# Kernel optimization log

Measured on AMD Instinct MI355X. Metric: run time of the kernel, lower is better.

## Reference

```python
import jax, jax.numpy as jnp
import numpy as np

DIM = 512
N = 131072


def _linear_params(key, dim):
    # torch nn.Linear default init: U(-1/sqrt(in), 1/sqrt(in)) for W and b
    kw, kb = jax.random.split(key)
    bound = 1.0 / np.sqrt(dim)
    W = jax.random.uniform(kw, (dim, dim), jnp.float32, -bound, bound)
    b = jax.random.uniform(kb, (dim,), jnp.float32, -bound, bound)
    return W, b


def setup_inputs() -> dict:
    key = jax.random.key(0)
    ks = jax.random.split(key, 8)
    x = jax.random.normal(ks[0], (N, DIM), jnp.float32)
    h = jax.random.normal(ks[1], (N, DIM), jnp.float32)
    W_rx, b_rx = _linear_params(ks[2], DIM)
    W_rh, b_rh = _linear_params(ks[3], DIM)
    W_zx, b_zx = _linear_params(ks[4], DIM)
    W_zh, b_zh = _linear_params(ks[5], DIM)
    W_nx, b_nx = _linear_params(ks[6], DIM)
    W_nh, b_nh = _linear_params(ks[7], DIM)
    return {
        "x": x, "h": h,
        "W_rx": W_rx, "b_rx": b_rx, "W_rh": W_rh, "b_rh": b_rh,
        "W_zx": W_zx, "b_zx": b_zx, "W_zh": W_zh, "b_zh": b_zh,
        "W_nx": W_nx, "b_nx": b_nx, "W_nh": W_nh, "b_nh": b_nh,
    }


def reference(x, h, W_rx, b_rx, W_rh, b_rh, W_zx, b_zx, W_zh, b_zh,
              W_nx, b_nx, W_nh, b_nh):
    # torch Linear: y = x @ W.T + b  (W stored [out, in])
    r = jax.nn.sigmoid(x @ W_rx.T + b_rx + h @ W_rh.T + b_rh)
    z = jax.nn.sigmoid(x @ W_zx.T + b_zx + h @ W_zh.T + b_zh)
    n = jnp.tanh(x @ W_nx.T + b_nx + (r * h) @ W_nh.T + b_nh)
    return (1.0 - z) * n + z * h
```

## Files before the change

### kernel.cpp

```cpp
#include <hip/hip_runtime.h>

#define DIM 512
#define NROWS 131072

typedef __attribute__((ext_vector_type(8))) __bf16 bf16x8;
typedef __attribute__((ext_vector_type(4))) float f32x4;

__device__ __forceinline__ unsigned short f2bf(float f) {
  unsigned u = __builtin_bit_cast(unsigned, f);
  return (unsigned short)((u + 0x7FFFu + ((u >> 16) & 1u)) >> 16);
}
__device__ __forceinline__ float bf2f(unsigned short u) {
  return __builtin_bit_cast(float, (unsigned)u << 16);
}

__device__ __forceinline__ f32x4 mfma16(bf16x8 a, bf16x8 b, f32x4 c) {
  return __builtin_amdgcn_mfma_f32_16x16x32_bf16(a, b, c, 0, 0, 0);
}

__device__ __forceinline__ float sigmoid_fast(float v) {
  return 1.0f / (1.0f + __expf(-v));
}
__device__ __forceinline__ float tanh_fast(float v) {
  float e = __expf(2.0f * v);
  return 1.0f - 2.0f / (e + 1.0f);
}

__device__ __forceinline__ void gl2lds(const unsigned char* g, unsigned char* l) {
  __builtin_amdgcn_global_load_lds(
      (const __attribute__((address_space(1))) unsigned int*)g,
      (__attribute__((address_space(3))) unsigned int*)l, 16, 0, 0);
}

__global__ void prepack_weights(const float* __restrict__ W0, const float* __restrict__ W1,
                                const float* __restrict__ W2, const float* __restrict__ W3,
                                const float* __restrict__ W4, const float* __restrict__ W5,
                                unsigned short* __restrict__ out) {
  int idx = blockIdx.x * 256 + threadIdx.x;
  int e = idx & 7;
  int l = (idx >> 3) & 63;
  int c = (idx >> 9) & 31;
  int f = (idx >> 14) & 15;
  int g = idx >> 18;
  const float* W = (g == 0) ? W0 : (g == 1) ? W1 : (g == 2) ? W2
                 : (g == 3) ? W3 : (g == 4) ? W4 : W5;
  int row = c * 16 + (l & 15);
  int kk  = f * 32 + ((l >> 4) << 3) + e;
  out[idx] = f2bf(W[row * DIM + kk]);
}

#define RH_OFF 65536
#define X_OFF  131072
#define LDS_BYTES 139264

__global__ __launch_bounds__(512, 1)
void gru_fused(const float* __restrict__ x, const float* __restrict__ h,
               const unsigned char* __restrict__ WB,
               const float* __restrict__ b_rx, const float* __restrict__ b_rh,
               const float* __restrict__ b_zx, const float* __restrict__ b_zh,
               const float* __restrict__ b_nx, const float* __restrict__ b_nh,
               float* __restrict__ out) {
  __shared__ __align__(1024) unsigned char lds[LDS_BYTES];

  const int tid  = threadIdx.x;
  const int lane = tid & 63;
  const int w    = tid >> 6;
  const int cfg0 = w * 4;
  const int row0 = blockIdx.x * 64;
  const int lr   = lane & 15;
  const int lk   = lane >> 4;

  auto stageChunk = [&](int g, int f, int dstOff) {
    const unsigned char* src = WB + (size_t)(g * 16 + f) * 32768;
#pragma unroll
    for (int it = 0; it < 4; ++it) {
      int o = (it * 512 + tid) * 16;
      gl2lds(src + o, &lds[dstOff + o]);
    }
  };

  float4 xreg;
  auto loadX = [&](int f) {
    int row = tid >> 3, kq = tid & 7;
    xreg = *(const float4*)(x + (size_t)(row0 + row) * DIM + f * 32 + kq * 4);
  };
  auto writeX = [&](int f) {
    int row = tid >> 3, kq = tid & 7;
    union { unsigned short us[4]; uint2 v; } p;
    p.us[0] = f2bf(xreg.x); p.us[1] = f2bf(xreg.y);
    p.us[2] = f2bf(xreg.z); p.us[3] = f2bf(xreg.w);
    *(uint2*)&lds[X_OFF + (f & 1) * 4096 + (row >> 4) * 1024
                  + ((kq >> 1) * 16 + (row & 15)) * 16 + (kq & 1) * 8] = p.v;
  };

  auto gateStage = [&](int abase, int bbase, f32x4 (&A)[4][4]) {
    bf16x8 af[4], bfr[4];
#pragma unroll
    for (int rf = 0; rf < 4; ++rf)
      af[rf] = *(const bf16x8*)&lds[abase + rf * 1024 + lane * 16];
#pragma unroll
    for (int cf = 0; cf < 4; ++cf)
      bfr[cf] = *(const bf16x8*)&lds[bbase + (cfg0 + cf) * 1024 + lane * 16];
#pragma unroll
    for (int rf = 0; rf < 4; ++rf)
#pragma unroll
      for (int cf = 0; cf < 4; ++cf)
        A[rf][cf] = mfma16(af[rf], bfr[cf], A[rf][cf]);
  };

  f32x4 accR[4][4] = {}, accZ[4][4] = {};

#pragma unroll
  for (int it = 0; it < 16; ++it) {
    int i = tid + it * 512;
    int row = i >> 7, kf4 = i & 127;
    int k = kf4 * 4;
    float4 hv4 = *(const float4*)(h + (size_t)(row0 + row) * DIM + k);
    union { unsigned short us[4]; uint2 v; } p;
    p.us[0] = f2bf(hv4.x); p.us[1] = f2bf(hv4.y);
    p.us[2] = f2bf(hv4.z); p.us[3] = f2bf(hv4.w);
    *(uint2*)&lds[(k >> 5) * 4096 + (row >> 4) * 1024
                  + (((k >> 3) & 3) * 16 + (row & 15)) * 16 + (k & 4) * 2] = p.v;
  }
  loadX(0); writeX(0);
  stageChunk(0, 0, RH_OFF);
  __syncthreads();

#pragma unroll 1
  for (int f = 0; f < 16; ++f) {
    const int xoff = X_OFF + (f & 1) * 4096;
    const int hoff = f * 4096;
    stageChunk(1, f, RH_OFF + 32768);
    if (f < 15) loadX(f + 1);
    gateStage(xoff, RH_OFF, accR);
    __syncthreads();
    stageChunk(2, f, RH_OFF);
    gateStage(xoff, RH_OFF + 32768, accZ);
    __syncthreads();
    stageChunk(3, f, RH_OFF + 32768);
    if (f < 15) writeX(f + 1);
    gateStage(hoff, RH_OFF, accR);
    __syncthreads();
    if (f < 15) stageChunk(0, f + 1, RH_OFF);
    gateStage(hoff, RH_OFF + 32768, accZ);
    __syncthreads();
  }

#pragma unroll
  for (int cf = 0; cf < 4; ++cf) {
    const int col  = (cfg0 + cf) * 16 + lr;
    const float bs = b_rx[col] + b_rh[col];
    const int fcol  = col >> 5;
    const int l2b   = ((col >> 3) & 3) * 16;
    const int ebyte = (col & 7) * 2;
#pragma unroll
    for (int rf = 0; rf < 4; ++rf) {
#pragma unroll
      for (int j = 0; j < 4; ++j) {
        const int rsub = lk * 4 + j;
        unsigned short hu = *(const unsigned short*)
            &lds[fcol * 4096 + rf * 1024 + (l2b + rsub) * 16 + ebyte];
        float rv = sigmoid_fast(accR[rf][cf][j] + bs);
        *(unsigned short*)
            &lds[RH_OFF + fcol * 4096 + rf * 1024 + (l2b + rsub) * 16 + ebyte]
            = f2bf(rv * bf2f(hu));
      }
    }
  }
  __syncthreads();

  f32x4 accN[4][4] = {};
  loadX(0); writeX(0);
  stageChunk(4, 0, 0);
  __syncthreads();
#pragma unroll 1
  for (int f = 0; f < 16; ++f) {
    const int xoff = X_OFF + (f & 1) * 4096;
    stageChunk(5, f, 32768);
    if (f < 15) loadX(f + 1);
    gateStage(xoff, 0, accN);
    __syncthreads();
    if (f < 15) { stageChunk(4, f + 1, 0); writeX(f + 1); }
    gateStage(RH_OFF + f * 4096, 32768, accN);
    __syncthreads();
  }

#pragma unroll
  for (int cf = 0; cf < 4; ++cf) {
    const int col  = (cfg0 + cf) * 16 + lr;
    const float bn = b_nx[col] + b_nh[col];
    const float bz = b_zx[col] + b_zh[col];
#pragma unroll
    for (int rf = 0; rf < 4; ++rf) {
#pragma unroll
      for (int j = 0; j < 4; ++j) {
        const int row = rf * 16 + lk * 4 + j;
        const size_t off = (size_t)(row0 + row) * DIM + col;
        float hv = h[off];
        float nv = tanh_fast(accN[rf][cf][j] + bn);
        float zv = sigmoid_fast(accZ[rf][cf][j] + bz);
        out[off] = (1.0f - zv) * nv + zv * hv;
      }
    }
  }
}

extern "C" void kernel_launch(void* const* d_in, const int* in_sizes, int n_in,
                              void* d_out, int out_size, void* d_ws, size_t ws_size,
                              hipStream_t stream) {
  const float* x    = (const float*)d_in[0];
  const float* h    = (const float*)d_in[1];
  const float* W_rx = (const float*)d_in[2];
  const float* b_rx = (const float*)d_in[3];
  const float* W_rh = (const float*)d_in[4];
  const float* b_rh = (const float*)d_in[5];
  const float* W_zx = (const float*)d_in[6];
  const float* b_zx = (const float*)d_in[7];
  const float* W_zh = (const float*)d_in[8];
  const float* b_zh = (const float*)d_in[9];
  const float* W_nx = (const float*)d_in[10];
  const float* b_nx = (const float*)d_in[11];
  const float* W_nh = (const float*)d_in[12];
  const float* b_nh = (const float*)d_in[13];

  unsigned short* wpack = (unsigned short*)d_ws;

  prepack_weights<<<6144, 256, 0, stream>>>(W_rx, W_zx, W_rh, W_zh, W_nx, W_nh, wpack);
  gru_fused<<<NROWS / 64, 512, 0, stream>>>(x, h, (const unsigned char*)wpack,
                                            b_rx, b_rh, b_zx, b_zh, b_nx, b_nh,
                                            (float*)d_out);
}
```

Before: 766.2 us.

## Split fused GRU into two tiled GEMM kernels with r*h workspace

Replaces the single fused kernel (64-row blocks, one block per CU, full weight restaging per block) with two conventional tiled GEMM kernels. The first computes the r and z gates over 128x128 output tiles with double-buffered LDS, XOR-swizzled fp32 A tiles and a grid swizzle. It writes r*h as bf16 to a workspace and z into the output buffer. The second computes n from x and the r*h workspace and combines it with z and h. This should raise occupancy and improve weight reuse, at the cost of extra global traffic for the r*h and z intermediates and fp32-to-bf16 conversion during LDS reads.

```diff
diff --git a/kernel.cpp b/kernel.cpp
--- a/kernel.cpp
+++ b/kernel.cpp
@@ -5,6 +5,8 @@
 
 typedef __attribute__((ext_vector_type(8))) __bf16 bf16x8;
 typedef __attribute__((ext_vector_type(4))) float f32x4;
+
+union BF8 { unsigned short us[8]; bf16x8 v; };
 
 __device__ __forceinline__ unsigned short f2bf(float f) {
   unsigned u = __builtin_bit_cast(unsigned, f);
@@ -47,6 +49,250 @@
   int row = c * 16 + (l & 15);
   int kk  = f * 32 + ((l >> 4) << 3) + e;
   out[idx] = f2bf(W[row * DIM + kk]);
+}
+
+
+__global__ __launch_bounds__(256, 3)
+void gemm_rz(const float* __restrict__ x, const float* __restrict__ h,
+             const unsigned char* __restrict__ WB,
+             const float* __restrict__ b_rx, const float* __restrict__ b_rh,
+             const float* __restrict__ b_zx, const float* __restrict__ b_zh,
+             unsigned short* __restrict__ rhws, float* __restrict__ zout) {
+  __shared__ __align__(1024) unsigned char ldsA[2][16384];
+  __shared__ __align__(1024) unsigned char ldsB[2][8192];
+
+  const int tid = threadIdx.x;
+  const int lane = tid & 63;
+  const int w = tid >> 6;
+  const int lr = lane & 15, lk = lane >> 4;
+  const int row0w = (w & 1) * 64;
+  const int cfw = (w >> 1) * 4;
+
+  const int bid = blockIdx.x;
+  const int swz = (bid & 7) * 1024 + (bid >> 3);
+  const int panel = swz >> 3;
+  const int n = swz & 7;
+  const int row0 = panel * 128;
+  const bool isR = (n < 4);
+  const int gx = isR ? 0 : 1, gh = isR ? 2 : 3;
+  const int c0 = (n & 3) * 8;
+
+  f32x4 acc[4][4] = {};
+
+  auto stageA = [&](int f, int buf) {
+    const float* src = (f < 16) ? x : h;
+    const int fk = f & 15;
+#pragma unroll
+    for (int it = 0; it < 4; ++it) {
+      int d = it * 4096 + tid * 16;
+      int row = d >> 7;
+      int u = (d >> 4) & 7;
+      const unsigned char* s =
+          (const unsigned char*)(src + (size_t)(row0 + row) * DIM + fk * 32)
+          + (((u ^ (row & 7)) & 7) << 4);
+      gl2lds(s, &ldsA[buf][d]);
+    }
+  };
+  auto stageB = [&](int g, int fk, int buf) {
+    const unsigned char* s = WB + ((size_t)((g * 16 + fk) * 32 + c0) << 10);
+#pragma unroll
+    for (int it = 0; it < 2; ++it) {
+      int d = it * 4096 + tid * 16;
+      gl2lds(s + d, &ldsB[buf][d]);
+    }
+  };
+  auto compute = [&](int buf) {
+    bf16x8 bfr[4], af[4];
+#pragma unroll
+    for (int cf = 0; cf < 4; ++cf)
+      bfr[cf] = *(const bf16x8*)&ldsB[buf][(cfw + cf) * 1024 + lane * 16];
+#pragma unroll
+    for (int rf = 0; rf < 4; ++rf) {
+      int rfr = row0w + rf * 16 + lr;
+      int u0 = lk * 2;
+      f32x4 a0 = *(const f32x4*)&ldsA[buf][rfr * 128 + (((u0) ^ (rfr & 7)) << 4)];
+      f32x4 a1 = *(const f32x4*)&ldsA[buf][rfr * 128 + (((u0 + 1) ^ (rfr & 7)) << 4)];
+      union { __bf16 e[8]; bf16x8 v; } cv;
+      cv.e[0] = (__bf16)a0[0]; cv.e[1] = (__bf16)a0[1];
+      cv.e[2] = (__bf16)a0[2]; cv.e[3] = (__bf16)a0[3];
+      cv.e[4] = (__bf16)a1[0]; cv.e[5] = (__bf16)a1[1];
+      cv.e[6] = (__bf16)a1[2]; cv.e[7] = (__bf16)a1[3];
+      af[rf] = cv.v;
+    }
+#pragma unroll
+    for (int rf = 0; rf < 4; ++rf)
+#pragma unroll
+      for (int cf = 0; cf < 4; ++cf)
+        acc[rf][cf] = mfma16(af[rf], bfr[cf], acc[rf][cf]);
+  };
+
+  stageA(0, 0); stageB(gx, 0, 0);
+  __syncthreads();
+#pragma unroll 1
+  for (int f = 0; f < 32; ++f) {
+    int buf = f & 1;
+    if (f < 31) {
+      int fn = f + 1;
+      stageA(fn, buf ^ 1);
+      stageB((fn < 16) ? gx : gh, fn & 15, buf ^ 1);
+    }
+    compute(buf);
+    __syncthreads();
+  }
+
+  const float* bx = isR ? b_rx : b_zx;
+  const float* bh = isR ? b_rh : b_zh;
+  const int coltile = (n & 3) * 128;
+#pragma unroll
+  for (int cf = 0; cf < 4; ++cf) {
+    int cg = coltile + (cfw + cf) * 16 + lr;
+    float bsum = bx[cg] + bh[cg];
+#pragma unroll
+    for (int rf = 0; rf < 4; ++rf) {
+#pragma unroll
+      for (int j = 0; j < 4; ++j) {
+        int row = row0 + row0w + rf * 16 + lk * 4 + j;
+        size_t off = (size_t)row * DIM + cg;
+        float v = acc[rf][cf][j] + bsum;
+        if (isR) {
+          float rv = sigmoid_fast(v);
+          rhws[off] = f2bf(rv * h[off]);
+        } else {
+          zout[off] = sigmoid_fast(v);
+        }
+      }
+    }
+  }
+}
+
+__global__ __launch_bounds__(256, 3)
+void gemm_n(const float* __restrict__ x, const float* __restrict__ h,
+            const unsigned char* __restrict__ WB,
+            const unsigned short* __restrict__ rhws,
+            const float* __restrict__ b_nx, const float* __restrict__ b_nh,
+            float* __restrict__ out) {
+  __shared__ __align__(1024) unsigned char ldsA[2][16384];
+  __shared__ __align__(1024) unsigned char ldsB[2][8192];
+
+  const int tid = threadIdx.x;
+  const int lane = tid & 63;
+  const int w = tid >> 6;
+  const int lr = lane & 15, lk = lane >> 4;
+  const int row0w = (w & 1) * 64;
+  const int cfw = (w >> 1) * 4;
+
+  const int bid = blockIdx.x;
+  const int swz = (bid & 7) * 512 + (bid >> 3);
+  const int panel = swz >> 2;
+  const int n = swz & 3;
+  const int row0 = panel * 128;
+  const int c0 = n * 8;
+
+  f32x4 acc[4][4] = {};
+
+  auto stageA = [&](int fk, int buf) {
+#pragma unroll
+    for (int it = 0; it < 4; ++it) {
+      int d = it * 4096 + tid * 16;
+      int row = d >> 7;
+      int u = (d >> 4) & 7;
+      const unsigned char* s =
+          (const unsigned char*)(x + (size_t)(row0 + row) * DIM + fk * 32)
+          + (((u ^ (row & 7)) & 7) << 4);
+      gl2lds(s, &ldsA[buf][d]);
+    }
+  };
+  auto stageRH = [&](int f2, int buf) {
+    const unsigned char* base = (const unsigned char*)rhws;
+#pragma unroll
+    for (int it = 0; it < 2; ++it) {
+      int d = it * 4096 + tid * 16;
+      int row = d >> 6;
+      int u = (d >> 4) & 3;
+      const unsigned char* s = base + (size_t)(row0 + row) * 1024 + f2 * 64
+                               + ((u ^ ((row >> 1) & 3)) << 4);
+      gl2lds(s, &ldsA[buf][d]);
+    }
+  };
+  auto stageB = [&](int g, int fk, int buf) {
+    const unsigned char* s = WB + ((size_t)((g * 16 + fk) * 32 + c0) << 10);
+#pragma unroll
+    for (int it = 0; it < 2; ++it) {
+      int d = it * 4096 + tid * 16;
+      gl2lds(s + d, &ldsB[buf][d]);
+    }
+  };
+  auto loadB = [&](int buf, bf16x8 (&bfr)[4]) {
+#pragma unroll
+    for (int cf = 0; cf < 4; ++cf)
+      bfr[cf] = *(const bf16x8*)&ldsB[buf][(cfw + cf) * 1024 + lane * 16];
+  };
+  auto domfma = [&](bf16x8 (&af)[4], bf16x8 (&bfr)[4]) {
+#pragma unroll
+    for (int rf = 0; rf < 4; ++rf)
+#pragma unroll
+      for (int cf = 0; cf < 4; ++cf)
+        acc[rf][cf] = mfma16(af[rf], bfr[cf], acc[rf][cf]);
+  };
+  auto computeX = [&](int buf) {
+    bf16x8 bfr[4], af[4];
+    loadB(buf, bfr);
+#pragma unroll
+    for (int rf = 0; rf < 4; ++rf) {
+      int rfr = row0w + rf * 16 + lr;
+      int u0 = lk * 2;
+      f32x4 a0 = *(const f32x4*)&ldsA[buf][rfr * 128 + (((u0) ^ (rfr & 7)) << 4)];
+      f32x4 a1 = *(const f32x4*)&ldsA[buf][rfr * 128 + (((u0 + 1) ^ (rfr & 7)) << 4)];
+      union { __bf16 e[8]; bf16x8 v; } cv;
+      cv.e[0] = (__bf16)a0[0]; cv.e[1] = (__bf16)a0[1];
+      cv.e[2] = (__bf16)a0[2]; cv.e[3] = (__bf16)a0[3];
+      cv.e[4] = (__bf16)a1[0]; cv.e[5] = (__bf16)a1[1];
+      cv.e[6] = (__bf16)a1[2]; cv.e[7] = (__bf16)a1[3];
+      af[rf] = cv.v;
+    }
+    domfma(af, bfr);
+  };
+  auto computeRH = [&](int buf) {
+    bf16x8 bfr[4], af[4];
+    loadB(buf, bfr);
+#pragma unroll
+    for (int rf = 0; rf < 4; ++rf) {
+      int rfr = row0w + rf * 16 + lr;
+      af[rf] = *(const bf16x8*)&ldsA[buf][rfr * 64 + ((lk ^ ((rfr >> 1) & 3)) << 4)];
+    }
+    domfma(af, bfr);
+  };
+
+  stageA(0, 0); stageB(4, 0, 0);
+  __syncthreads();
+#pragma unroll 1
+  for (int f = 0; f < 32; ++f) {
+    int buf = f & 1;
+    if (f < 31) {
+      int fn = f + 1;
+      if (fn < 16) { stageA(fn, buf ^ 1);      stageB(4, fn, buf ^ 1); }
+      else         { stageRH(fn - 16, buf ^ 1); stageB(5, fn - 16, buf ^ 1); }
+    }
+    if (f < 16) computeX(buf); else computeRH(buf);
+    __syncthreads();
+  }
+
+#pragma unroll
+  for (int cf = 0; cf < 4; ++cf) {
+    int cg = n * 128 + (cfw + cf) * 16 + lr;
+    float bsum = b_nx[cg] + b_nh[cg];
+#pragma unroll
+    for (int rf = 0; rf < 4; ++rf) {
+#pragma unroll
+      for (int j = 0; j < 4; ++j) {
+        int row = row0 + row0w + rf * 16 + lk * 4 + j;
+        size_t off = (size_t)row * DIM + cg;
+        float nv = tanh_fast(acc[rf][cf][j] + bsum);
+        float zv = out[off];
+        out[off] = (1.0f - zv) * nv + zv * h[off];
+      }
+    }
+  }
 }
 
 #define RH_OFF 65536
@@ -223,10 +469,22 @@
   const float* W_nh = (const float*)d_in[12];
   const float* b_nh = (const float*)d_in[13];
 
-  unsigned short* wpack = (unsigned short*)d_ws;
+  unsigned char* ws = (unsigned char*)d_ws;
+  unsigned short* wpack = (unsigned short*)ws;
 
   prepack_weights<<<6144, 256, 0, stream>>>(W_rx, W_zx, W_rh, W_zh, W_nx, W_nh, wpack);
-  gru_fused<<<NROWS / 64, 512, 0, stream>>>(x, h, (const unsigned char*)wpack,
-                                            b_rx, b_rh, b_zx, b_zh, b_nx, b_nh,
-                                            (float*)d_out);
-}
+
+  const size_t need = (4ull << 20) + (size_t)NROWS * DIM * 2;
+  if (ws_size >= need) {
+    unsigned short* rhws = (unsigned short*)(ws + (4ull << 20));
+    gemm_rz<<<8192, 256, 0, stream>>>(x, h, (const unsigned char*)wpack,
+                                      b_rx, b_rh, b_zx, b_zh,
+                                      rhws, (float*)d_out);
+    gemm_n<<<4096, 256, 0, stream>>>(x, h, (const unsigned char*)wpack,
+                                     rhws, b_nx, b_nh, (float*)d_out);
+  } else {
+    gru_fused<<<NROWS / 64, 512, 0, stream>>>(x, h, (const unsigned char*)wpack,
+                                              b_rx, b_rh, b_zx, b_zh, b_nx, b_nh,
+                                              (float*)d_out);
+  }
+}
```

New measurement: 1.178 ms. 1.54x slower.

## Pre-convert x to bf16 and stream it via async LDS loads with vmcnt waits

Applied to the files above, without the earlier changes.

A new pre-kernel converts x to bf16 in workspace, and the main kernel stages x tiles straight into LDS with global_load_lds in pairs of k-chunks, instead of a register load, convert and LDS write. The __syncthreads calls are replaced by explicit s_waitcnt vmcnt counts plus bare s_barrier, so weight and x loads can stay in flight across barriers. The aim is to take x conversion and register round-trips off the critical path and overlap loads with MFMA work. In exchange it adds an extra pass over x (read fp32, write bf16) and relies on fragile hand-counted vmcnt values.

```diff
diff --git a/kernel.cpp b/kernel.cpp
--- a/kernel.cpp
+++ b/kernel.cpp
@@ -26,7 +26,7 @@
   return 1.0f - 2.0f / (e + 1.0f);
 }
 
-__device__ __forceinline__ void gl2lds(const unsigned char* g, unsigned char* l) {
+__device__ __forceinline__ void gl2lds(const void* g, void* l) {
   __builtin_amdgcn_global_load_lds(
       (const __attribute__((address_space(1))) unsigned int*)g,
       (__attribute__((address_space(3))) unsigned int*)l, 16, 0, 0);
@@ -49,12 +49,23 @@
   out[idx] = f2bf(W[row * DIM + kk]);
 }
 
-#define RH_OFF 65536
-#define X_OFF  131072
-#define LDS_BYTES 139264
+__global__ void prep_x(const float* __restrict__ x, unsigned short* __restrict__ xb) {
+  size_t i = (size_t)(blockIdx.x * 256 + threadIdx.x) * 8;
+  float4 a0 = *(const float4*)(x + i);
+  float4 a1 = *(const float4*)(x + i + 4);
+  union { unsigned short us[8]; uint4 v; } p;
+  p.us[0] = f2bf(a0.x); p.us[1] = f2bf(a0.y); p.us[2] = f2bf(a0.z); p.us[3] = f2bf(a0.w);
+  p.us[4] = f2bf(a1.x); p.us[5] = f2bf(a1.y); p.us[6] = f2bf(a1.z); p.us[7] = f2bf(a1.w);
+  *(uint4*)(xb + i) = p.v;
+}
+
+#define BOFF 65536
+#define XOFF 131072
+#define LDS_BYTES 147456
 
 __global__ __launch_bounds__(512, 1)
 void gru_fused(const float* __restrict__ x, const float* __restrict__ h,
+               const unsigned short* __restrict__ xb,
                const unsigned char* __restrict__ WB,
                const float* __restrict__ b_rx, const float* __restrict__ b_rh,
                const float* __restrict__ b_zx, const float* __restrict__ b_zh,
@@ -70,29 +81,20 @@
   const int lr   = lane & 15;
   const int lk   = lane >> 4;
 
-  auto stageChunk = [&](int g, int f, int dstOff) {
+  auto stageB = [&](int g, int f, int dst) {
     const unsigned char* src = WB + (size_t)(g * 16 + f) * 32768;
 #pragma unroll
     for (int it = 0; it < 4; ++it) {
       int o = (it * 512 + tid) * 16;
-      gl2lds(src + o, &lds[dstOff + o]);
+      gl2lds(src + o, &lds[dst + o]);
     }
   };
-
-  float4 xreg;
-  auto loadX = [&](int f) {
-    int row = tid >> 3, kq = tid & 7;
-    xreg = *(const float4*)(x + (size_t)(row0 + row) * DIM + f * 32 + kq * 4);
+  auto stageXpair = [&](int p) {
+    int fh = tid >> 8, rf = (tid >> 6) & 3, l = tid & 63;
+    const unsigned short* src = xb + (size_t)(row0 + rf * 16 + (l & 15)) * DIM
+                                + p * 64 + fh * 32 + (l >> 4) * 8;
+    gl2lds(src, &lds[XOFF + (p & 1) * 8192 + tid * 16]);
   };
-  auto writeX = [&](int f) {
-    int row = tid >> 3, kq = tid & 7;
-    union { unsigned short us[4]; uint2 v; } p;
-    p.us[0] = f2bf(xreg.x); p.us[1] = f2bf(xreg.y);
-    p.us[2] = f2bf(xreg.z); p.us[3] = f2bf(xreg.w);
-    *(uint2*)&lds[X_OFF + (f & 1) * 4096 + (row >> 4) * 1024
-                  + ((kq >> 1) * 16 + (row & 15)) * 16 + (kq & 1) * 8] = p.v;
-  };
-
   auto gateStage = [&](int abase, int bbase, f32x4 (&A)[4][4]) {
     bf16x8 af[4], bfr[4];
 #pragma unroll
@@ -113,8 +115,8 @@
 #pragma unroll
   for (int it = 0; it < 16; ++it) {
     int i = tid + it * 512;
-    int row = i >> 7, kf4 = i & 127;
-    int k = kf4 * 4;
+    int row = i >> 7;
+    int k = (i & 127) * 4;
     float4 hv4 = *(const float4*)(h + (size_t)(row0 + row) * DIM + k);
     union { unsigned short us[4]; uint2 v; } p;
     p.us[0] = f2bf(hv4.x); p.us[1] = f2bf(hv4.y);
@@ -122,28 +124,44 @@
     *(uint2*)&lds[(k >> 5) * 4096 + (row >> 4) * 1024
                   + (((k >> 3) & 3) * 16 + (row & 15)) * 16 + (k & 4) * 2] = p.v;
   }
-  loadX(0); writeX(0);
-  stageChunk(0, 0, RH_OFF);
+  stageXpair(0);
+  stageB(0, 0, BOFF);
   __syncthreads();
 
 #pragma unroll 1
   for (int f = 0; f < 16; ++f) {
-    const int xoff = X_OFF + (f & 1) * 4096;
-    const int hoff = f * 4096;
-    stageChunk(1, f, RH_OFF + 32768);
-    if (f < 15) loadX(f + 1);
-    gateStage(xoff, RH_OFF, accR);
-    __syncthreads();
-    stageChunk(2, f, RH_OFF);
-    gateStage(xoff, RH_OFF + 32768, accZ);
-    __syncthreads();
-    stageChunk(3, f, RH_OFF + 32768);
-    if (f < 15) writeX(f + 1);
-    gateStage(hoff, RH_OFF, accR);
-    __syncthreads();
-    if (f < 15) stageChunk(0, f + 1, RH_OFF);
-    gateStage(hoff, RH_OFF + 32768, accZ);
-    __syncthreads();
+    const int xo = XOFF + ((f >> 1) & 1) * 8192 + (f & 1) * 4096;
+    const int ho = f * 4096;
+    stageB(1, f, BOFF + 32768);
+    if (f & 1) {
+      int p1 = (f >> 1) + 1; if (p1 > 7) p1 = 7;
+      stageXpair(p1);
+      asm volatile("s_waitcnt vmcnt(5)" ::: "memory");
+    } else {
+      asm volatile("s_waitcnt vmcnt(4)" ::: "memory");
+    }
+    __builtin_amdgcn_s_barrier();
+    gateStage(xo, BOFF, accR);
+    __builtin_amdgcn_s_barrier();
+    stageB(2, f, BOFF);
+    asm volatile("s_waitcnt vmcnt(4)" ::: "memory");
+    __builtin_amdgcn_s_barrier();
+    gateStage(xo, BOFF + 32768, accZ);
+    __builtin_amdgcn_s_barrier();
+    stageB(3, f, BOFF + 32768);
+    asm volatile("s_waitcnt vmcnt(4)" ::: "memory");
+    __builtin_amdgcn_s_barrier();
+    gateStage(ho, BOFF, accR);
+    __builtin_amdgcn_s_barrier();
+    if (f < 15) {
+      stageB(0, f + 1, BOFF);
+      asm volatile("s_waitcnt vmcnt(4)" ::: "memory");
+    } else {
+      asm volatile("s_waitcnt vmcnt(0)" ::: "memory");
+    }
+    __builtin_amdgcn_s_barrier();
+    gateStage(ho, BOFF + 32768, accZ);
+    __builtin_amdgcn_s_barrier();
   }
 
 #pragma unroll
@@ -162,7 +180,7 @@
             &lds[fcol * 4096 + rf * 1024 + (l2b + rsub) * 16 + ebyte];
         float rv = sigmoid_fast(accR[rf][cf][j] + bs);
         *(unsigned short*)
-            &lds[RH_OFF + fcol * 4096 + rf * 1024 + (l2b + rsub) * 16 + ebyte]
+            &lds[BOFF + fcol * 4096 + rf * 1024 + (l2b + rsub) * 16 + ebyte]
             = f2bf(rv * bf2f(hu));
       }
     }
@@ -170,19 +188,31 @@
   __syncthreads();
 
   f32x4 accN[4][4] = {};
-  loadX(0); writeX(0);
-  stageChunk(4, 0, 0);
-  __syncthreads();
+  stageXpair(0);
+  stageB(4, 0, 0);
 #pragma unroll 1
   for (int f = 0; f < 16; ++f) {
-    const int xoff = X_OFF + (f & 1) * 4096;
-    stageChunk(5, f, 32768);
-    if (f < 15) loadX(f + 1);
-    gateStage(xoff, 0, accN);
-    __syncthreads();
-    if (f < 15) { stageChunk(4, f + 1, 0); writeX(f + 1); }
-    gateStage(RH_OFF + f * 4096, 32768, accN);
-    __syncthreads();
+    const int xo = XOFF + ((f >> 1) & 1) * 8192 + (f & 1) * 4096;
+    stageB(5, f, 32768);
+    if (f & 1) {
+      int p1 = (f >> 1) + 1; if (p1 > 7) p1 = 7;
+      stageXpair(p1);
+      asm volatile("s_waitcnt vmcnt(5)" ::: "memory");
+    } else {
+      asm volatile("s_waitcnt vmcnt(4)" ::: "memory");
+    }
+    __builtin_amdgcn_s_barrier();
+    gateStage(xo, 0, accN);
+    __builtin_amdgcn_s_barrier();
+    if (f < 15) {
+      stageB(4, f + 1, 0);
+      asm volatile("s_waitcnt vmcnt(4)" ::: "memory");
+    } else {
+      asm volatile("s_waitcnt vmcnt(0)" ::: "memory");
+    }
+    __builtin_amdgcn_s_barrier();
+    gateStage(BOFF + f * 4096, 32768, accN);
+    __builtin_amdgcn_s_barrier();
   }
 
 #pragma unroll
@@ -223,10 +253,13 @@
   const float* W_nh = (const float*)d_in[12];
   const float* b_nh = (const float*)d_in[13];
 
-  unsigned short* wpack = (unsigned short*)d_ws;
+  unsigned char* ws = (unsigned char*)d_ws;
+  unsigned short* wpack = (unsigned short*)ws;
+  unsigned short* xb    = (unsigned short*)(ws + (4ull << 20));
 
   prepack_weights<<<6144, 256, 0, stream>>>(W_rx, W_zx, W_rh, W_zh, W_nx, W_nh, wpack);
-  gru_fused<<<NROWS / 64, 512, 0, stream>>>(x, h, (const unsigned char*)wpack,
+  prep_x<<<32768, 256, 0, stream>>>(x, xb);
+  gru_fused<<<NROWS / 64, 512, 0, stream>>>(x, h, xb, (const unsigned char*)wpack,
                                             b_rx, b_rh, b_zx, b_zh, b_nx, b_nh,
                                             (float*)d_out);
 }
```

After: 671.1 us. 1.14x faster.

## Load weights directly to registers, pre-convert x to bf16, drop LDS staging

Applied to the files above, without the earlier changes.

Weight fragments are now read from global memory straight into registers in a software-pipelined loop instead of being staged through LDS with barriers. x is converted to bf16 by a separate prep kernel and loaded directly as MFMA A fragments. LDS shrinks to 64KB (h only, reused in place for r*h) so two blocks can share a CU, and the per-step syncthreads are removed. The cost is an extra pass over x in a separate kernel, plus every wave reading its own weight slice from L2 rather than sharing a staged copy.

```diff
diff --git a/kernel.cpp b/kernel.cpp
--- a/kernel.cpp
+++ b/kernel.cpp
@@ -24,12 +24,6 @@
 __device__ __forceinline__ float tanh_fast(float v) {
   float e = __expf(2.0f * v);
   return 1.0f - 2.0f / (e + 1.0f);
-}
-
-__device__ __forceinline__ void gl2lds(const unsigned char* g, unsigned char* l) {
-  __builtin_amdgcn_global_load_lds(
-      (const __attribute__((address_space(1))) unsigned int*)g,
-      (__attribute__((address_space(3))) unsigned int*)l, 16, 0, 0);
 }
 
 __global__ void prepack_weights(const float* __restrict__ W0, const float* __restrict__ W1,
@@ -49,72 +43,69 @@
   out[idx] = f2bf(W[row * DIM + kk]);
 }
 
-#define RH_OFF 65536
-#define X_OFF  131072
-#define LDS_BYTES 139264
-
-__global__ __launch_bounds__(512, 1)
-void gru_fused(const float* __restrict__ x, const float* __restrict__ h,
+__global__ void prep_x(const float* __restrict__ x, unsigned short* __restrict__ xb) {
+  size_t i = (size_t)(blockIdx.x * 256 + threadIdx.x) * 8;
+  float4 a0 = *(const float4*)(x + i);
+  float4 a1 = *(const float4*)(x + i + 4);
+  union { unsigned short us[8]; uint4 v; } p;
+  p.us[0] = f2bf(a0.x); p.us[1] = f2bf(a0.y); p.us[2] = f2bf(a0.z); p.us[3] = f2bf(a0.w);
+  p.us[4] = f2bf(a1.x); p.us[5] = f2bf(a1.y); p.us[6] = f2bf(a1.z); p.us[7] = f2bf(a1.w);
+  *(uint4*)(xb + i) = p.v;
+}
+
+__global__ __launch_bounds__(512, 2)
+void gru_fused(const float* __restrict__ h,
+               const unsigned short* __restrict__ xb,
                const unsigned char* __restrict__ WB,
                const float* __restrict__ b_rx, const float* __restrict__ b_rh,
                const float* __restrict__ b_zx, const float* __restrict__ b_zh,
                const float* __restrict__ b_nx, const float* __restrict__ b_nh,
                float* __restrict__ out) {
-  __shared__ __align__(1024) unsigned char lds[LDS_BYTES];
+  __shared__ __align__(1024) unsigned char lds[65536];
 
   const int tid  = threadIdx.x;
   const int lane = tid & 63;
   const int w    = tid >> 6;
-  const int cfg0 = w * 4;
   const int row0 = blockIdx.x * 64;
   const int lr   = lane & 15;
   const int lk   = lane >> 4;
-
-  auto stageChunk = [&](int g, int f, int dstOff) {
-    const unsigned char* src = WB + (size_t)(g * 16 + f) * 32768;
-#pragma unroll
-    for (int it = 0; it < 4; ++it) {
-      int o = (it * 512 + tid) * 16;
-      gl2lds(src + o, &lds[dstOff + o]);
-    }
+  const int boff = w * 4096 + lane * 16;
+
+  auto loadB = [&](int g, int f, bf16x8 (&b)[4]) {
+    const unsigned char* p = WB + (((size_t)(g * 16 + f)) << 15) + boff;
+#pragma unroll
+    for (int cf = 0; cf < 4; ++cf)
+      b[cf] = *(const bf16x8*)(p + cf * 1024);
   };
-
-  float4 xreg;
-  auto loadX = [&](int f) {
-    int row = tid >> 3, kq = tid & 7;
-    xreg = *(const float4*)(x + (size_t)(row0 + row) * DIM + f * 32 + kq * 4);
+  auto loadXA = [&](int f, bf16x8 (&a)[4]) {
+#pragma unroll
+    for (int rf = 0; rf < 4; ++rf)
+      a[rf] = *(const bf16x8*)(xb + (size_t)(row0 + rf * 16 + lr) * DIM
+                               + f * 32 + lk * 8);
   };
-  auto writeX = [&](int f) {
-    int row = tid >> 3, kq = tid & 7;
-    union { unsigned short us[4]; uint2 v; } p;
-    p.us[0] = f2bf(xreg.x); p.us[1] = f2bf(xreg.y);
-    p.us[2] = f2bf(xreg.z); p.us[3] = f2bf(xreg.w);
-    *(uint2*)&lds[X_OFF + (f & 1) * 4096 + (row >> 4) * 1024
-                  + ((kq >> 1) * 16 + (row & 15)) * 16 + (kq & 1) * 8] = p.v;
+  auto readLDS = [&](int f, bf16x8 (&a)[4]) {
+#pragma unroll
+    for (int rf = 0; rf < 4; ++rf)
+      a[rf] = *(const bf16x8*)&lds[f * 4096 + rf * 1024 + lane * 16];
   };
 
-  auto gateStage = [&](int abase, int bbase, f32x4 (&A)[4][4]) {
-    bf16x8 af[4], bfr[4];
-#pragma unroll
-    for (int rf = 0; rf < 4; ++rf)
-      af[rf] = *(const bf16x8*)&lds[abase + rf * 1024 + lane * 16];
-#pragma unroll
-    for (int cf = 0; cf < 4; ++cf)
-      bfr[cf] = *(const bf16x8*)&lds[bbase + (cfg0 + cf) * 1024 + lane * 16];
-#pragma unroll
-    for (int rf = 0; rf < 4; ++rf)
-#pragma unroll
-      for (int cf = 0; cf < 4; ++cf)
-        A[rf][cf] = mfma16(af[rf], bfr[cf], A[rf][cf]);
-  };
-
-  f32x4 accR[4][4] = {}, accZ[4][4] = {};
-
+#define WINDOW(Aset, Bset, ACC)                                                \
+  _Pragma("unroll")                                                            \
+  for (int rf_ = 0; rf_ < 4; ++rf_)                                            \
+    _Pragma("unroll")                                                          \
+    for (int cf_ = 0; cf_ < 4; ++cf_)                                          \
+      ACC[rf_][cf_] = mfma16(Aset[rf_], Bset[cf_], ACC[rf_][cf_]);
+
+  bf16x8 bA[4], bB[4], xaC[4], xaN[4], ha[4];
+
+  loadB(0, 0, bA);
+  loadB(1, 0, bB);
+  loadXA(0, xaC);
 #pragma unroll
   for (int it = 0; it < 16; ++it) {
     int i = tid + it * 512;
-    int row = i >> 7, kf4 = i & 127;
-    int k = kf4 * 4;
+    int row = i >> 7;
+    int k = (i & 127) * 4;
     float4 hv4 = *(const float4*)(h + (size_t)(row0 + row) * DIM + k);
     union { unsigned short us[4]; uint2 v; } p;
     p.us[0] = f2bf(hv4.x); p.us[1] = f2bf(hv4.y);
@@ -122,72 +113,69 @@
     *(uint2*)&lds[(k >> 5) * 4096 + (row >> 4) * 1024
                   + (((k >> 3) & 3) * 16 + (row & 15)) * 16 + (k & 4) * 2] = p.v;
   }
-  loadX(0); writeX(0);
-  stageChunk(0, 0, RH_OFF);
   __syncthreads();
 
+  f32x4 accR[4][4] = {}, accZ[4][4] = {};
 #pragma unroll 1
   for (int f = 0; f < 16; ++f) {
-    const int xoff = X_OFF + (f & 1) * 4096;
-    const int hoff = f * 4096;
-    stageChunk(1, f, RH_OFF + 32768);
-    if (f < 15) loadX(f + 1);
-    gateStage(xoff, RH_OFF, accR);
-    __syncthreads();
-    stageChunk(2, f, RH_OFF);
-    gateStage(xoff, RH_OFF + 32768, accZ);
-    __syncthreads();
-    stageChunk(3, f, RH_OFF + 32768);
-    if (f < 15) writeX(f + 1);
-    gateStage(hoff, RH_OFF, accR);
-    __syncthreads();
-    if (f < 15) stageChunk(0, f + 1, RH_OFF);
-    gateStage(hoff, RH_OFF + 32768, accZ);
-    __syncthreads();
-  }
+    const int fn = (f < 15) ? f + 1 : 15;
+    readLDS(f, ha);
+    WINDOW(xaC, bA, accR);
+    loadB(2, f, bA);
+    WINDOW(xaC, bB, accZ);
+    loadB(3, f, bB);
+    loadXA(fn, xaN);
+    WINDOW(ha, bA, accR);
+    loadB(0, fn, bA);
+    WINDOW(ha, bB, accZ);
+    loadB(1, fn, bB);
+#pragma unroll
+    for (int rf = 0; rf < 4; ++rf) xaC[rf] = xaN[rf];
+  }
+
+  loadB(4, 0, bA);
+  loadB(5, 0, bB);
+  loadXA(0, xaC);
+  __syncthreads();
 
 #pragma unroll
   for (int cf = 0; cf < 4; ++cf) {
-    const int col  = (cfg0 + cf) * 16 + lr;
+    const int col  = (w * 4 + cf) * 16 + lr;
     const float bs = b_rx[col] + b_rh[col];
-    const int fcol  = col >> 5;
-    const int l2b   = ((col >> 3) & 3) * 16;
-    const int ebyte = (col & 7) * 2;
+    const int fcol = col >> 5;
+    const int l2b  = ((col >> 3) & 3) * 16;
+    const int eb   = (col & 7) * 2;
 #pragma unroll
     for (int rf = 0; rf < 4; ++rf) {
 #pragma unroll
       for (int j = 0; j < 4; ++j) {
         const int rsub = lk * 4 + j;
-        unsigned short hu = *(const unsigned short*)
-            &lds[fcol * 4096 + rf * 1024 + (l2b + rsub) * 16 + ebyte];
+        const int addr = fcol * 4096 + rf * 1024 + (l2b + rsub) * 16 + eb;
+        unsigned short hu = *(const unsigned short*)&lds[addr];
         float rv = sigmoid_fast(accR[rf][cf][j] + bs);
-        *(unsigned short*)
-            &lds[RH_OFF + fcol * 4096 + rf * 1024 + (l2b + rsub) * 16 + ebyte]
-            = f2bf(rv * bf2f(hu));
+        *(unsigned short*)&lds[addr] = f2bf(rv * bf2f(hu));
       }
     }
   }
   __syncthreads();
 
   f32x4 accN[4][4] = {};
-  loadX(0); writeX(0);
-  stageChunk(4, 0, 0);
-  __syncthreads();
 #pragma unroll 1
   for (int f = 0; f < 16; ++f) {
-    const int xoff = X_OFF + (f & 1) * 4096;
-    stageChunk(5, f, 32768);
-    if (f < 15) loadX(f + 1);
-    gateStage(xoff, 0, accN);
-    __syncthreads();
-    if (f < 15) { stageChunk(4, f + 1, 0); writeX(f + 1); }
-    gateStage(RH_OFF + f * 4096, 32768, accN);
-    __syncthreads();
+    const int fn = (f < 15) ? f + 1 : 15;
+    readLDS(f, ha);
+    WINDOW(xaC, bA, accN);
+    loadB(4, fn, bA);
+    loadXA(fn, xaN);
+    WINDOW(ha, bB, accN);
+    loadB(5, fn, bB);
+#pragma unroll
+    for (int rf = 0; rf < 4; ++rf) xaC[rf] = xaN[rf];
   }
 
 #pragma unroll
   for (int cf = 0; cf < 4; ++cf) {
-    const int col  = (cfg0 + cf) * 16 + lr;
+    const int col  = (w * 4 + cf) * 16 + lr;
     const float bn = b_nx[col] + b_nh[col];
     const float bz = b_zx[col] + b_zh[col];
 #pragma unroll
@@ -203,6 +191,7 @@
       }
     }
   }
+#undef WINDOW
 }
 
 extern "C" void kernel_launch(void* const* d_in, const int* in_sizes, int n_in,
@@ -223,10 +212,13 @@
   const float* W_nh = (const float*)d_in[12];
   const float* b_nh = (const float*)d_in[13];
 
-  unsigned short* wpack = (unsigned short*)d_ws;
+  unsigned char* ws = (unsigned char*)d_ws;
+  unsigned short* wpack = (unsigned short*)ws;
+  unsigned short* xb    = (unsigned short*)(ws + (4ull << 20));
 
   prepack_weights<<<6144, 256, 0, stream>>>(W_rx, W_zx, W_rh, W_zh, W_nx, W_nh, wpack);
-  gru_fused<<<NROWS / 64, 512, 0, stream>>>(x, h, (const unsigned char*)wpack,
+  prep_x<<<32768, 256, 0, stream>>>(x, xb);
+  gru_fused<<<NROWS / 64, 512, 0, stream>>>(h, xb, (const unsigned char*)wpack,
                                             b_rx, b_rh, b_zx, b_zh, b_nx, b_nh,
                                             (float*)d_out);
 }
```

Measured after the change: 726.2 us. -5.2%, faster.
